# Optimization experiments

Hardware: AMD Instinct MI355X
Metric: run time of the kernel (lower is better)

Reference implementation:

```python
import jax, jax.numpy as jnp
import numpy as np

EPS = 1e-16

def _householder_cascade(vectors):
    # vectors: [N, S, 1]
    v = vectors[..., 0]                                  # [N, S]
    outer = jnp.einsum('ns,nt->nst', v, v)               # [N, S, S]
    inner = jnp.sum(v * v, axis=-1)[:, None, None]       # [N, 1, 1]
    S = v.shape[-1]
    I = jnp.eye(S, dtype=vectors.dtype)
    hh = I[None] - 2.0 * outer / (inner + EPS)           # [N, S, S]
    # sequential left-to-right product: Q = H_0 @ H_1 @ ... @ H_{N-1}
    def step(Q, M):
        return Q @ M, None
    Q, _ = jax.lax.scan(step, I, hh)
    return Q

def setup_inputs() -> dict:
    key = jax.random.key(0)
    k1, k2 = jax.random.split(key)
    S, N, B = 256, 258, 65536
    vectors = jax.random.normal(k1, (N, S, 1), dtype=jnp.float32)
    vectors = vectors / jnp.linalg.norm(vectors, axis=1, keepdims=True)
    x = jax.random.normal(k2, (B, S), dtype=jnp.float32)
    return {"x": x, "vectors": vectors}

def reference(x, vectors):
    Q = _householder_cascade(vectors)   # [S, S]
    return x @ Q.T
```

## Files before the change

kernel.cpp:

```cpp
#include <hip/hip_runtime.h>


#define GLOAD_LDS16(g, l)                                                      \
  __builtin_amdgcn_global_load_lds(                                            \
      (const __attribute__((address_space(1))) void*)(g),                      \
      (__attribute__((address_space(3))) void*)(l), 16, 0, 0)

typedef __attribute__((ext_vector_type(8))) short bf16x8;
typedef __attribute__((ext_vector_type(4))) float f32x4;

__device__ __forceinline__ unsigned short f2bf_rne(float f) {
  unsigned u = __builtin_bit_cast(unsigned, f);
  return (unsigned short)((u + 0x7fffu + ((u >> 16) & 1u)) >> 16);
}

template <int CTRL>
__device__ __forceinline__ float dpp_add(float v) {
  int t = __builtin_amdgcn_update_dpp(0, __builtin_bit_cast(int, v), CTRL, 0xF,
                                      0xF, true);
  return v + __builtin_bit_cast(float, t);
}

__device__ __forceinline__ float dpp_sum16(float p) {
  p = dpp_add<0xB1>(p);
  p = dpp_add<0x4E>(p);
  p = dpp_add<0x124>(p);
  p = dpp_add<0x128>(p);
  return p;
}

__launch_bounds__(64, 1)
__global__ void hh_qchunk(const float* __restrict__ vecs,
                          float* __restrict__ Qc) {
  const int l = threadIdx.x;
  const int chunk = blockIdx.x >> 6;
  const int rg = blockIdx.x & 63;
  const int r = l >> 4;
  const int cl = l & 15;
  const int row = rg * 4 + r;
  const int col0 = cl * 16;
  const int brow = chunk * 33;

  __shared__ float cs[36];

  for (int n = r; n < 36; n += 4) {
    const int gr = brow + n;
    const int grc = gr > 257 ? 257 : gr;
    const float4* vp = (const float4*)(vecs + (long)grc * 256 + col0);
    float s = 0.f;
#pragma unroll
    for (int i = 0; i < 4; ++i) {
      float4 t = vp[i];
      s += t.x * t.x + t.y * t.y + t.z * t.z + t.w * t.w;
    }
    s = dpp_sum16(s);
    if (cl == 0)
      cs[n] = (n < 33 && gr < 258) ? 2.0f / (s + 1e-16f) : 0.f;
  }
  __syncthreads();

  float q[16];
#pragma unroll
  for (int i = 0; i < 16; ++i) q[i] = (col0 + i == row) ? 1.f : 0.f;

  auto load16 = [&](float(&d)[16], int n) {
    const int gr = brow + n;
    const int grc = gr > 257 ? 257 : gr;
    const float4* v = (const float4*)(vecs + (long)grc * 256 + col0);
#pragma unroll
    for (int i = 0; i < 4; ++i) {
      float4 t = v[i];
      d[4 * i] = t.x; d[4 * i + 1] = t.y; d[4 * i + 2] = t.z; d[4 * i + 3] = t.w;
    }
  };

  auto step = [&](const float(&a)[16], float cc) {
    float p0 = 0.f, p1 = 0.f, p2 = 0.f, p3 = 0.f;
#pragma unroll
    for (int e = 0; e < 4; ++e) {
      p0 = fmaf(q[e], a[e], p0);
      p1 = fmaf(q[4 + e], a[4 + e], p1);
      p2 = fmaf(q[8 + e], a[8 + e], p2);
      p3 = fmaf(q[12 + e], a[12 + e], p3);
    }
    float p = dpp_sum16((p0 + p1) + (p2 + p3));
    const float s = cc * p;
#pragma unroll
    for (int k = 0; k < 16; ++k) q[k] = fmaf(-s, a[k], q[k]);
  };

  float A0[16], A1[16];
  load16(A0, 0);
  load16(A1, 1);
  float c0 = cs[0], c1 = cs[1];
  for (int n = 0; n < 32; n += 2) {
    const float cn0 = cs[n + 2], cn1 = cs[n + 3];
    step(A0, c0);
    load16(A0, n + 2);
    step(A1, c1);
    load16(A1, n + 3);
    c0 = cn0; c1 = cn1;
  }
  step(A0, c0);

  float4* out = (float4*)(Qc + (long)chunk * 65536 + row * 256 + col0);
#pragma unroll
  for (int i = 0; i < 4; ++i)
    out[i] = make_float4(q[4 * i], q[4 * i + 1], q[4 * i + 2], q[4 * i + 3]);
}

__launch_bounds__(256)
__global__ void hh_mm(const float* __restrict__ in, float* __restrict__ out,
                      unsigned short* __restrict__ outb, int to_bf16) {
  const int b = blockIdx.x >> 6;
  const int t = blockIdx.x & 63;
  const int ti = (t >> 3) * 32, tj = (t & 7) * 32;
  const int tid = threadIdx.x;
  const int tx = tid & 15, ty = tid >> 4;
  const float* A = in + (long)b * 2 * 65536;
  const float* Bm = A + 65536;

  __shared__ float As[32][68];
  __shared__ float Bs[64][36];

  float acc00 = 0.f, acc01 = 0.f, acc10 = 0.f, acc11 = 0.f;

  for (int k0 = 0; k0 < 256; k0 += 64) {
#pragma unroll
    for (int u0 = 0; u0 < 2048; u0 += 1024) {
      int idx = u0 + tid * 4;
      int rr = idx >> 6, cc = idx & 63;
      *(float4*)&As[rr][cc] = *(const float4*)&A[(ti + rr) * 256 + k0 + cc];
      int kk = idx >> 5, jj = idx & 31;
      *(float4*)&Bs[kk][jj] = *(const float4*)&Bm[(k0 + kk) * 256 + tj + jj];
    }
    __syncthreads();
#pragma unroll 8
    for (int kk = 0; kk < 64; ++kk) {
      float a0 = As[2 * ty][kk], a1 = As[2 * ty + 1][kk];
      float b0 = Bs[kk][2 * tx], b1 = Bs[kk][2 * tx + 1];
      acc00 = fmaf(a0, b0, acc00);
      acc01 = fmaf(a0, b1, acc01);
      acc10 = fmaf(a1, b0, acc10);
      acc11 = fmaf(a1, b1, acc11);
    }
    __syncthreads();
  }

  const int gi = ti + 2 * ty, gj = tj + 2 * tx;
  if (to_bf16) {
    unsigned short* o = outb + (long)b * 65536;
    o[gi * 256 + gj] = f2bf_rne(acc00);
    o[gi * 256 + gj + 1] = f2bf_rne(acc01);
    o[(gi + 1) * 256 + gj] = f2bf_rne(acc10);
    o[(gi + 1) * 256 + gj + 1] = f2bf_rne(acc11);
  } else {
    float* o = out + (long)b * 65536;
    o[gi * 256 + gj] = acc00;
    o[gi * 256 + gj + 1] = acc01;
    o[(gi + 1) * 256 + gj] = acc10;
    o[(gi + 1) * 256 + gj + 1] = acc11;
  }
}

__launch_bounds__(512)
__global__ void hh_gemm(const float* __restrict__ X,
                        const unsigned short* __restrict__ Qb,
                        float* __restrict__ Y) {
  __shared__ __align__(128) char lds[65536];
  const int tid = threadIdx.x;
  const int lane = tid & 63;
  const int wid = tid >> 6;
  const int wm = wid >> 2;
  const int wn = wid & 3;
  const int fr = lane & 15;
  const int fg = lane >> 4;
  const long bm0 = (long)blockIdx.x * 128;

  auto stage = [&](int buf, int kt) {
#pragma unroll
    for (int r2 = 0; r2 < 2; ++r2) {
      int slot = r2 * 512 + tid;
      int row = slot >> 3, seg = slot & 7;
      int ps = seg ^ (row & 7);
      GLOAD_LDS16(X + (bm0 + row) * 256 + kt * 32 + ps * 4,
                  lds + buf * 16384 + slot * 16);
    }
#pragma unroll
    for (int r2 = 0; r2 < 2; ++r2) {
      int slot = r2 * 512 + tid;
      int row = slot >> 2, seg = slot & 3;
      int ps = seg ^ (row & 3);
      GLOAD_LDS16(Qb + row * 256 + kt * 32 + ps * 8,
                  lds + 32768 + buf * 16384 + slot * 16);
    }
  };

  f32x4 acc[4][4];
#pragma unroll
  for (int m = 0; m < 4; ++m)
#pragma unroll
    for (int n = 0; n < 4; ++n) acc[m][n] = (f32x4){0.f, 0.f, 0.f, 0.f};

  stage(0, 0);
  __syncthreads();

  for (int kt = 0; kt < 8; ++kt) {
    const int cur = kt & 1;
    if (kt < 7) stage(cur ^ 1, kt + 1);

    bf16x8 aF[4], bF[4];
#pragma unroll
    for (int m = 0; m < 4; ++m) {
      int row = wm * 64 + m * 16 + fr;
      int s0 = (2 * fg) ^ (row & 7);
      int s1 = (2 * fg + 1) ^ (row & 7);
      const f32x4 x0 = *(const f32x4*)(lds + cur * 16384 + row * 128 + s0 * 16);
      const f32x4 x1 = *(const f32x4*)(lds + cur * 16384 + row * 128 + s1 * 16);
      bf16x8 t;
      t[0] = (short)f2bf_rne(x0[0]);
      t[1] = (short)f2bf_rne(x0[1]);
      t[2] = (short)f2bf_rne(x0[2]);
      t[3] = (short)f2bf_rne(x0[3]);
      t[4] = (short)f2bf_rne(x1[0]);
      t[5] = (short)f2bf_rne(x1[1]);
      t[6] = (short)f2bf_rne(x1[2]);
      t[7] = (short)f2bf_rne(x1[3]);
      aF[m] = t;
    }
#pragma unroll
    for (int n = 0; n < 4; ++n) {
      int row = wn * 64 + n * 16 + fr;
      int ps = fg ^ (row & 3);
      bF[n] = *(const bf16x8*)(lds + 32768 + cur * 16384 + row * 64 + ps * 16);
    }
#pragma unroll
    for (int m = 0; m < 4; ++m)
#pragma unroll
      for (int n = 0; n < 4; ++n)
        acc[m][n] =
            __builtin_amdgcn_mfma_f32_16x16x32_bf16(aF[m], bF[n], acc[m][n], 0, 0, 0);
    __syncthreads();
  }

#pragma unroll
  for (int m = 0; m < 4; ++m)
#pragma unroll
    for (int n = 0; n < 4; ++n)
#pragma unroll
      for (int r = 0; r < 4; ++r) {
        long grow = bm0 + wm * 64 + m * 16 + fg * 4 + r;
        int gcol = wn * 64 + n * 16 + fr;
        Y[grow * 256 + gcol] = acc[m][n][r];
      }
}

extern "C" void kernel_launch(void* const* d_in, const int* in_sizes, int n_in,
                              void* d_out, int out_size, void* d_ws, size_t ws_size,
                              hipStream_t stream) {
  const float* x = (const float*)d_in[0];
  const float* vecs = (const float*)d_in[1];
  float* y = (float*)d_out;

  unsigned short* Qb = (unsigned short*)d_ws;

  char* ob = (char*)d_out;
  float* Qc = (float*)(ob);
  float* P = (float*)(ob + 2097152);
  float* R = (float*)(ob + 3145728);

  hh_qchunk<<<512, 64, 0, stream>>>(vecs, Qc);
  hh_mm<<<256, 256, 0, stream>>>(Qc, P, nullptr, 0);
  hh_mm<<<128, 256, 0, stream>>>(P, R, nullptr, 0);
  hh_mm<<<64, 256, 0, stream>>>(R, nullptr, Qb, 1);
  hh_gemm<<<512, 512, 0, stream>>>(x, Qb, y);
}
```

Measured before the change: 62.77 us.

## Use two 129-reflector chunks instead of eight, dropping two merge matmul launches

The Householder product is now built from 2 chunks of 129 reflectors each (128 blocks) instead of 8 chunks of 33 (512 blocks). Only one chunk-merge matmul is then needed, so two small hh_mm launches and their intermediate buffers go away. In exchange, each qchunk block runs a serial chain four times longer and the grid is a quarter the size, which uses far fewer CUs and lengthens the critical path of the first kernel.

New measurement: 74.56 us. 1.19x slower.

```diff
diff --git a/kernel.cpp b/kernel.cpp
--- a/kernel.cpp
+++ b/kernel.cpp
@@ -39,24 +39,22 @@
   const int cl = l & 15;
   const int row = rg * 4 + r;
   const int col0 = cl * 16;
-  const int brow = chunk * 33;
-
-  __shared__ float cs[36];
-
-  for (int n = r; n < 36; n += 4) {
-    const int gr = brow + n;
-    const int grc = gr > 257 ? 257 : gr;
-    const float4* vp = (const float4*)(vecs + (long)grc * 256 + col0);
+  const int brow = chunk * 129;
+
+  __shared__ float cs[132];
+
+  for (int n = r; n < 129; n += 4) {
+    const f32x4* vp = (const f32x4*)(vecs + (long)(brow + n) * 256 + col0);
     float s = 0.f;
 #pragma unroll
     for (int i = 0; i < 4; ++i) {
-      float4 t = vp[i];
-      s += t.x * t.x + t.y * t.y + t.z * t.z + t.w * t.w;
+      f32x4 t = vp[i];
+      s += t[0] * t[0] + t[1] * t[1] + t[2] * t[2] + t[3] * t[3];
     }
     s = dpp_sum16(s);
-    if (cl == 0)
-      cs[n] = (n < 33 && gr < 258) ? 2.0f / (s + 1e-16f) : 0.f;
-  }
+    if (cl == 0) cs[n] = 2.0f / (s + 1e-16f);
+  }
+  if (l < 3) cs[129 + l] = 0.f;
   __syncthreads();
 
   float q[16];
@@ -64,9 +62,9 @@
   for (int i = 0; i < 16; ++i) q[i] = (col0 + i == row) ? 1.f : 0.f;
 
   auto load16 = [&](float(&d)[16], int n) {
-    const int gr = brow + n;
-    const int grc = gr > 257 ? 257 : gr;
-    const float4* v = (const float4*)(vecs + (long)grc * 256 + col0);
+    int gr = brow + n;
+    gr = gr > 257 ? 257 : gr;
+    const float4* v = (const float4*)(vecs + (long)gr * 256 + col0);
 #pragma unroll
     for (int i = 0; i < 4; ++i) {
       float4 t = v[i];
@@ -83,7 +81,7 @@
       p2 = fmaf(q[8 + e], a[8 + e], p2);
       p3 = fmaf(q[12 + e], a[12 + e], p3);
     }
-    float p = dpp_sum16((p0 + p1) + (p2 + p3));
+    const float p = dpp_sum16((p0 + p1) + (p2 + p3));
     const float s = cc * p;
 #pragma unroll
     for (int k = 0; k < 16; ++k) q[k] = fmaf(-s, a[k], q[k]);
@@ -93,7 +91,7 @@
   load16(A0, 0);
   load16(A1, 1);
   float c0 = cs[0], c1 = cs[1];
-  for (int n = 0; n < 32; n += 2) {
+  for (int n = 0; n < 128; n += 2) {
     const float cn0 = cs[n + 2], cn1 = cs[n + 3];
     step(A0, c0);
     load16(A0, n + 2);
@@ -110,15 +108,14 @@
 }
 
 __launch_bounds__(256)
-__global__ void hh_mm(const float* __restrict__ in, float* __restrict__ out,
-                      unsigned short* __restrict__ outb, int to_bf16) {
-  const int b = blockIdx.x >> 6;
-  const int t = blockIdx.x & 63;
+__global__ void hh_mm(const float* __restrict__ in,
+                      unsigned short* __restrict__ outb) {
+  const int t = blockIdx.x;
   const int ti = (t >> 3) * 32, tj = (t & 7) * 32;
   const int tid = threadIdx.x;
   const int tx = tid & 15, ty = tid >> 4;
-  const float* A = in + (long)b * 2 * 65536;
-  const float* Bm = A + 65536;
+  const float* A = in;
+  const float* Bm = in + 65536;
 
   __shared__ float As[32][68];
   __shared__ float Bs[64][36];
@@ -148,19 +145,10 @@
   }
 
   const int gi = ti + 2 * ty, gj = tj + 2 * tx;
-  if (to_bf16) {
-    unsigned short* o = outb + (long)b * 65536;
-    o[gi * 256 + gj] = f2bf_rne(acc00);
-    o[gi * 256 + gj + 1] = f2bf_rne(acc01);
-    o[(gi + 1) * 256 + gj] = f2bf_rne(acc10);
-    o[(gi + 1) * 256 + gj + 1] = f2bf_rne(acc11);
-  } else {
-    float* o = out + (long)b * 65536;
-    o[gi * 256 + gj] = acc00;
-    o[gi * 256 + gj + 1] = acc01;
-    o[(gi + 1) * 256 + gj] = acc10;
-    o[(gi + 1) * 256 + gj + 1] = acc11;
-  }
+  outb[gi * 256 + gj] = f2bf_rne(acc00);
+  outb[gi * 256 + gj + 1] = f2bf_rne(acc01);
+  outb[(gi + 1) * 256 + gj] = f2bf_rne(acc10);
+  outb[(gi + 1) * 256 + gj + 1] = f2bf_rne(acc11);
 }
 
 __launch_bounds__(512)
@@ -263,15 +251,9 @@
   float* y = (float*)d_out;
 
   unsigned short* Qb = (unsigned short*)d_ws;
-
-  char* ob = (char*)d_out;
-  float* Qc = (float*)(ob);
-  float* P = (float*)(ob + 2097152);
-  float* R = (float*)(ob + 3145728);
-
-  hh_qchunk<<<512, 64, 0, stream>>>(vecs, Qc);
-  hh_mm<<<256, 256, 0, stream>>>(Qc, P, nullptr, 0);
-  hh_mm<<<128, 256, 0, stream>>>(P, R, nullptr, 0);
-  hh_mm<<<64, 256, 0, stream>>>(R, nullptr, Qb, 1);
+  float* Qc = (float*)d_out;
+
+  hh_qchunk<<<128, 64, 0, stream>>>(vecs, Qc);
+  hh_mm<<<64, 256, 0, stream>>>(Qc, Qb);
   hh_gemm<<<512, 512, 0, stream>>>(x, Qb, y);
 }
```

## Merge chunk Q products into one split-bf16 MFMA kernel

Applied to the files above, without the earlier changes.

The three tree-reduction fp32 FMA matmul launches are replaced by a single kernel. Each block holds a 16-row strip of the running product and multiplies it sequentially through the 7 remaining chunk matrices using bf16 hi/lo split MFMAs (three products per step) to approximate fp32 accuracy. The chunk kernel now also writes transposed hi/lo bf16 copies of each chunk Q. This cuts two launches and moves the Q-chain work onto matrix cores, but only 16 blocks run a longer sequential chain and read B operands straight from global memory, and the split-bf16 scheme drops the lo*lo term, which costs some precision.

Result: slower. 98.18 us, median of 2 (+56.4%).

```diff
diff --git a/kernel.cpp b/kernel.cpp
--- a/kernel.cpp
+++ b/kernel.cpp
@@ -12,6 +12,17 @@
 __device__ __forceinline__ unsigned short f2bf_rne(float f) {
   unsigned u = __builtin_bit_cast(unsigned, f);
   return (unsigned short)((u + 0x7fffu + ((u >> 16) & 1u)) >> 16);
+}
+
+struct bfpair { unsigned short hi, lo; };
+
+__device__ __forceinline__ bfpair bf_split(float x) {
+  unsigned short hu = f2bf_rne(x);
+  float hf = __builtin_bit_cast(float, (unsigned)hu << 16);
+  bfpair r;
+  r.hi = hu;
+  r.lo = f2bf_rne(x - hf);
+  return r;
 }
 
 template <int CTRL>
@@ -31,7 +42,9 @@
 
 __launch_bounds__(64, 1)
 __global__ void hh_qchunk(const float* __restrict__ vecs,
-                          float* __restrict__ Qc) {
+                          float* __restrict__ Qc,
+                          unsigned short* __restrict__ QcTh,
+                          unsigned short* __restrict__ QcTl) {
   const int l = threadIdx.x;
   const int chunk = blockIdx.x >> 6;
   const int rg = blockIdx.x & 63;
@@ -54,8 +67,7 @@
       s += t.x * t.x + t.y * t.y + t.z * t.z + t.w * t.w;
     }
     s = dpp_sum16(s);
-    if (cl == 0)
-      cs[n] = (n < 33 && gr < 258) ? 2.0f / (s + 1e-16f) : 0.f;
+    if (cl == 0) cs[n] = (n < 33 && gr < 258) ? 2.0f / (s + 1e-16f) : 0.f;
   }
   __syncthreads();
 
@@ -70,7 +82,8 @@
 #pragma unroll
     for (int i = 0; i < 4; ++i) {
       float4 t = v[i];
-      d[4 * i] = t.x; d[4 * i + 1] = t.y; d[4 * i + 2] = t.z; d[4 * i + 3] = t.w;
+      d[4 * i] = t.x; d[4 * i + 1] = t.y;
+      d[4 * i + 2] = t.z; d[4 * i + 3] = t.w;
     }
   };
 
@@ -83,7 +96,7 @@
       p2 = fmaf(q[8 + e], a[8 + e], p2);
       p3 = fmaf(q[12 + e], a[12 + e], p3);
     }
-    float p = dpp_sum16((p0 + p1) + (p2 + p3));
+    const float p = dpp_sum16((p0 + p1) + (p2 + p3));
     const float s = cc * p;
 #pragma unroll
     for (int k = 0; k < 16; ++k) q[k] = fmaf(-s, a[k], q[k]);
@@ -107,59 +120,81 @@
 #pragma unroll
   for (int i = 0; i < 4; ++i)
     out[i] = make_float4(q[4 * i], q[4 * i + 1], q[4 * i + 2], q[4 * i + 3]);
+  unsigned short* oth = QcTh + (long)chunk * 65536 + row;
+  unsigned short* otl = QcTl + (long)chunk * 65536 + row;
+#pragma unroll
+  for (int i = 0; i < 16; ++i) {
+    bfpair p = bf_split(q[i]);
+    oth[(col0 + i) * 256] = p.hi;
+    otl[(col0 + i) * 256] = p.lo;
+  }
 }
 
 __launch_bounds__(256)
-__global__ void hh_mm(const float* __restrict__ in, float* __restrict__ out,
-                      unsigned short* __restrict__ outb, int to_bf16) {
-  const int b = blockIdx.x >> 6;
-  const int t = blockIdx.x & 63;
-  const int ti = (t >> 3) * 32, tj = (t & 7) * 32;
+__global__ void hh_qmerge(const float* __restrict__ Qc,
+                          const unsigned short* __restrict__ QcTh,
+                          const unsigned short* __restrict__ QcTl,
+                          unsigned short* __restrict__ Qb) {
+  __shared__ __align__(16) unsigned short CurHi[16][264];
+  __shared__ __align__(16) unsigned short CurLo[16][264];
   const int tid = threadIdx.x;
-  const int tx = tid & 15, ty = tid >> 4;
-  const float* A = in + (long)b * 2 * 65536;
-  const float* Bm = A + 65536;
-
-  __shared__ float As[32][68];
-  __shared__ float Bs[64][36];
-
-  float acc00 = 0.f, acc01 = 0.f, acc10 = 0.f, acc11 = 0.f;
-
-  for (int k0 = 0; k0 < 256; k0 += 64) {
-#pragma unroll
-    for (int u0 = 0; u0 < 2048; u0 += 1024) {
-      int idx = u0 + tid * 4;
-      int rr = idx >> 6, cc = idx & 63;
-      *(float4*)&As[rr][cc] = *(const float4*)&A[(ti + rr) * 256 + k0 + cc];
-      int kk = idx >> 5, jj = idx & 31;
-      *(float4*)&Bs[kk][jj] = *(const float4*)&Bm[(k0 + kk) * 256 + tj + jj];
+  const int lane = tid & 63, w = tid >> 6;
+  const int fr = lane & 15, fg = lane >> 4;
+  const int rb = blockIdx.x * 16;
+
+  {
+    const int rr = tid >> 4, c0 = (tid & 15) * 16;
+    const float* src = Qc + (long)(rb + rr) * 256 + c0;
+#pragma unroll
+    for (int i = 0; i < 16; ++i) {
+      bfpair p = bf_split(src[i]);
+      CurHi[rr][c0 + i] = p.hi;
+      CurLo[rr][c0 + i] = p.lo;
+    }
+  }
+  __syncthreads();
+
+  for (int prod = 1; prod < 8; ++prod) {
+    const unsigned short* BTh = QcTh + (long)prod * 65536;
+    const unsigned short* BTl = QcTl + (long)prod * 65536;
+    f32x4 acc[4];
+#pragma unroll
+    for (int n = 0; n < 4; ++n) acc[n] = (f32x4){0.f, 0.f, 0.f, 0.f};
+
+    for (int kt = 0; kt < 8; ++kt) {
+      const int k0 = kt * 32 + fg * 8;
+      const bf16x8 aHi = *(const bf16x8*)&CurHi[fr][k0];
+      const bf16x8 aLo = *(const bf16x8*)&CurLo[fr][k0];
+#pragma unroll
+      for (int n = 0; n < 4; ++n) {
+        const long bcol = w * 64 + n * 16 + fr;
+        const bf16x8 bHi = *(const bf16x8*)(BTh + bcol * 256 + k0);
+        const bf16x8 bLo = *(const bf16x8*)(BTl + bcol * 256 + k0);
+        acc[n] = __builtin_amdgcn_mfma_f32_16x16x32_bf16(aHi, bHi, acc[n], 0, 0, 0);
+        acc[n] = __builtin_amdgcn_mfma_f32_16x16x32_bf16(aHi, bLo, acc[n], 0, 0, 0);
+        acc[n] = __builtin_amdgcn_mfma_f32_16x16x32_bf16(aLo, bHi, acc[n], 0, 0, 0);
+      }
     }
     __syncthreads();
-#pragma unroll 8
-    for (int kk = 0; kk < 64; ++kk) {
-      float a0 = As[2 * ty][kk], a1 = As[2 * ty + 1][kk];
-      float b0 = Bs[kk][2 * tx], b1 = Bs[kk][2 * tx + 1];
-      acc00 = fmaf(a0, b0, acc00);
-      acc01 = fmaf(a0, b1, acc01);
-      acc10 = fmaf(a1, b0, acc10);
-      acc11 = fmaf(a1, b1, acc11);
-    }
-    __syncthreads();
-  }
-
-  const int gi = ti + 2 * ty, gj = tj + 2 * tx;
-  if (to_bf16) {
-    unsigned short* o = outb + (long)b * 65536;
-    o[gi * 256 + gj] = f2bf_rne(acc00);
-    o[gi * 256 + gj + 1] = f2bf_rne(acc01);
-    o[(gi + 1) * 256 + gj] = f2bf_rne(acc10);
-    o[(gi + 1) * 256 + gj + 1] = f2bf_rne(acc11);
-  } else {
-    float* o = out + (long)b * 65536;
-    o[gi * 256 + gj] = acc00;
-    o[gi * 256 + gj + 1] = acc01;
-    o[(gi + 1) * 256 + gj] = acc10;
-    o[(gi + 1) * 256 + gj + 1] = acc11;
+
+    if (prod < 7) {
+#pragma unroll
+      for (int n = 0; n < 4; ++n)
+#pragma unroll
+        for (int rr = 0; rr < 4; ++rr) {
+          bfpair p = bf_split(acc[n][rr]);
+          CurHi[fg * 4 + rr][w * 64 + n * 16 + fr] = p.hi;
+          CurLo[fg * 4 + rr][w * 64 + n * 16 + fr] = p.lo;
+        }
+      __syncthreads();
+    } else {
+#pragma unroll
+      for (int n = 0; n < 4; ++n)
+#pragma unroll
+        for (int rr = 0; rr < 4; ++rr)
+          Qb[(long)(rb + fg * 4 + rr) * 256 + w * 64 + n * 16 + fr] =
+              f2bf_rne(acc[n][rr]);
+    }
   }
 }
 
@@ -266,12 +301,10 @@
 
   char* ob = (char*)d_out;
   float* Qc = (float*)(ob);
-  float* P = (float*)(ob + 2097152);
-  float* R = (float*)(ob + 3145728);
-
-  hh_qchunk<<<512, 64, 0, stream>>>(vecs, Qc);
-  hh_mm<<<256, 256, 0, stream>>>(Qc, P, nullptr, 0);
-  hh_mm<<<128, 256, 0, stream>>>(P, R, nullptr, 0);
-  hh_mm<<<64, 256, 0, stream>>>(R, nullptr, Qb, 1);
+  unsigned short* QcTh = (unsigned short*)(ob + 2097152);
+  unsigned short* QcTl = (unsigned short*)(ob + 3145728);
+
+  hh_qchunk<<<512, 64, 0, stream>>>(vecs, Qc, QcTh, QcTl);
+  hh_qmerge<<<16, 256, 0, stream>>>(Qc, QcTh, QcTl, Qb);
   hh_gemm<<<512, 512, 0, stream>>>(x, Qb, y);
 }
```
